# Performance work log

Hardware: AMD Instinct MI355X
Metric: run time of the kernel (lower is better)

## Reference

```python
import jax, jax.numpy as jnp
import numpy as np

H = 1024          # hiddenSize
V = 50257         # outputSize (vocab)
L = 512           # maxLength (encoder length)


def setup_inputs() -> dict:
    key = jax.random.key(0)
    ks = jax.random.split(key, 16)
    s = 0.02
    return {
        "input": jax.random.randint(ks[0], (1,), 0, V),
        "hidden": jax.random.normal(ks[1], (1, 1, H), jnp.float32),
        "encoder_outputs": jax.random.normal(ks[2], (L, H), jnp.float32),
        "emb": jax.random.normal(ks[3], (V, H), jnp.float32) * s,
        "W_attn": jax.random.normal(ks[4], (L, 2 * H), jnp.float32) * s,
        "b_attn": jnp.zeros((L,), jnp.float32),
        "W_comb": jax.random.normal(ks[5], (H, 2 * H), jnp.float32) * s,
        "b_comb": jnp.zeros((H,), jnp.float32),
        "W_ih": jax.random.normal(ks[6], (3 * H, H), jnp.float32) * s,
        "W_hh": jax.random.normal(ks[7], (3 * H, H), jnp.float32) * s,
        "b_ih": jnp.zeros((3 * H,), jnp.float32),
        "b_hh": jnp.zeros((3 * H,), jnp.float32),
        "W_out": jax.random.normal(ks[8], (V, H), jnp.float32) * s,
        "b_out": jnp.zeros((V,), jnp.float32),
    }


def reference(input, hidden, encoder_outputs, emb, W_attn, b_attn,
              W_comb, b_comb, W_ih, W_hh, b_ih, b_hh, W_out, b_out):
    # embedding lookup: [1, H] (dropout p=0 -> identity)
    embedded = emb[input]
    h = hidden[0]                                   # [1, H]
    # attention over encoder positions
    attn_logits = jnp.concatenate([embedded, h], axis=1) @ W_attn.T + b_attn
    attn_weights = jax.nn.softmax(attn_logits, axis=1)      # [1, L]
    attn_applied = attn_weights @ encoder_outputs           # [1, H]
    # combine and relu
    x = jnp.concatenate([embedded, attn_applied], axis=1) @ W_comb.T + b_comb
    x = jax.nn.relu(x)                                      # [1, H]
    # single GRU step (PyTorch gate layout: r, z, n)
    gi = x @ W_ih.T + b_ih                                  # [1, 3H]
    gh = h @ W_hh.T + b_hh                                  # [1, 3H]
    i_r, i_z, i_n = jnp.split(gi, 3, axis=1)
    h_r, h_z, h_n = jnp.split(gh, 3, axis=1)
    r = jax.nn.sigmoid(i_r + h_r)
    z = jax.nn.sigmoid(i_z + h_z)
    n = jnp.tanh(i_n + r * h_n)
    h_new = (1.0 - z) * n + z * h                           # [1, H]
    # output distribution
    output = jax.nn.log_softmax(h_new @ W_out.T + b_out, axis=1)  # [1, V]
    return output, h_new[None], attn_weights
```

## Files before the change

kernel.cpp:

```cpp
#include <hip/hip_runtime.h>
#include <cmath>

#define H 1024
#define V 50257
#define L 512
#define NB5 1571
#define NPART 128

__device__ __forceinline__ float wred_sum(float v) {
#pragma unroll
    for (int o = 32; o > 0; o >>= 1) v += __shfl_xor(v, o, 64);
    return v;
}
__device__ __forceinline__ float dot4(float4 a, float4 b) {
    return a.x * b.x + a.y * b.y + a.z * b.z + a.w * b.w;
}
__device__ __forceinline__ void ms_merge(float& m, float& s, float m2, float s2) {
    float M = fmaxf(m, m2);
    if (M == -INFINITY) { m = M; s = 0.f; return; }
    s = s * expf(m - M) + s2 * expf(m2 - M);
    m = M;
}

__global__ void k_phase1(const int* __restrict__ tok,
                         const float* __restrict__ hid,
                         const float* __restrict__ emb,
                         const float* __restrict__ Wa,
                         const float* __restrict__ ba,
                         const float* __restrict__ enc,
                         const float* __restrict__ Whh,
                         const float* __restrict__ bhh,
                         float* __restrict__ elg,
                         float* __restrict__ pbuf,
                         float* __restrict__ gh) {
    const int t = threadIdx.x, lane = t & 63, wv = t >> 6, b = blockIdx.x;
    const float4* h4 = (const float4*)hid;
    if (b < NPART) {
        const int l = b * 4 + wv;
        const float4* e4 = (const float4*)(emb + (size_t)tok[0] * H);
        const float4* wr = (const float4*)(Wa + (size_t)l * 2048);
        float acc = 0.f;
#pragma unroll
        for (int k = 0; k < 8; ++k) {
            int f = 64 * k + lane;
            float4 s = (f < 256) ? e4[f] : h4[f - 256];
            acc += dot4(wr[f], s);
        }
        acc = wred_sum(acc);
        const float e = expf(acc + ba[l]);
        __shared__ float se[4];
        if (lane == 0) { se[wv] = e; elg[l] = e; }
        __syncthreads();
        float4 a = make_float4(0.f, 0.f, 0.f, 0.f);
#pragma unroll
        for (int r = 0; r < 4; ++r) {
            const float w = se[r];
            const float4 v = ((const float4*)(enc + (size_t)(b * 4 + r) * H))[t];
            a.x += w * v.x; a.y += w * v.y; a.z += w * v.z; a.w += w * v.w;
        }
        ((float4*)pbuf)[b * 256 + t] = a;
    } else {
        const int base = (b - NPART) * 12 + wv * 3;
#pragma unroll
        for (int r = 0; r < 3; ++r) {
            const int j = base + r;
            const float4* wh = (const float4*)(Whh + (size_t)j * H);
            float acc = 0.f;
#pragma unroll
            for (int k = 0; k < 4; ++k) {
                int f = 64 * k + lane;
                acc += dot4(wh[f], h4[f]);
            }
            acc = wred_sum(acc);
            if (lane == 0) gh[j] = acc + bhh[j];
        }
    }
}

__global__ void k_comb(const int* __restrict__ tok,
                       const float* __restrict__ emb,
                       const float* __restrict__ elg,
                       const float* __restrict__ pbuf,
                       const float* __restrict__ Wc,
                       const float* __restrict__ bcb,
                       float* __restrict__ xv,
                       float* __restrict__ wout) {
    const int t = threadIdx.x, lane = t & 63, wv = t >> 6, b = blockIdx.x;
    __shared__ float red[4];
    __shared__ float4 aaL[256];
    const float e0 = elg[t], e1 = elg[t + 256];
    float s = wred_sum(e0 + e1);
    if (lane == 0) red[wv] = s;
    __syncthreads();
    const float invS = 1.f / (red[0] + red[1] + red[2] + red[3]);
    float4 a = make_float4(0.f, 0.f, 0.f, 0.f);
#pragma unroll 8
    for (int i = 0; i < NPART; ++i) {
        const float4 p = ((const float4*)pbuf)[i * 256 + t];
        a.x += p.x; a.y += p.y; a.z += p.z; a.w += p.w;
    }
    a.x *= invS; a.y *= invS; a.z *= invS; a.w *= invS;
    aaL[t] = a;
    __syncthreads();
    if (b == 0) { wout[t] = e0 * invS; wout[t + 256] = e1 * invS; }
    const int j = b * 4 + wv;
    const float4* e4 = (const float4*)(emb + (size_t)tok[0] * H);
    const float4* wr = (const float4*)(Wc + (size_t)j * 2048);
    float acc = 0.f;
#pragma unroll
    for (int k = 0; k < 4; ++k) {
        int f = 64 * k + lane;
        acc += dot4(wr[f], e4[f]);
        acc += dot4(wr[256 + f], aaL[f]);
    }
    acc = wred_sum(acc);
    if (lane == 0) xv[j] = fmaxf(acc + bcb[j], 0.f);
}

__global__ void k_gates_gru(const float* __restrict__ xv,
                            const float* __restrict__ hid,
                            const float* __restrict__ Wih,
                            const float* __restrict__ bih,
                            const float* __restrict__ gh,
                            float* __restrict__ hn_out,
                            float* __restrict__ hn_ws) {
    const int lane = threadIdx.x & 63, wv = threadIdx.x >> 6;
    const int j = blockIdx.x * 4 + wv;
    const float4* x4 = (const float4*)xv;
    float4 xreg[4];
#pragma unroll
    for (int k = 0; k < 4; ++k) xreg[k] = x4[64 * k + lane];
    float g[3];
#pragma unroll
    for (int p = 0; p < 3; ++p) {
        const float4* wr = (const float4*)(Wih + (size_t)(j + p * H) * H);
        float acc = 0.f;
#pragma unroll
        for (int k = 0; k < 4; ++k) acc += dot4(wr[64 * k + lane], xreg[k]);
        g[p] = wred_sum(acc) + bih[j + p * H];
    }
    if (lane == 0) {
        float r = 1.f / (1.f + expf(-(g[0] + gh[j])));
        float z = 1.f / (1.f + expf(-(g[1] + gh[j + H])));
        float n = tanhf(g[2] + r * gh[j + 2 * H]);
        float hv = (1.f - z) * n + z * hid[j];
        hn_out[j] = hv;
        hn_ws[j] = hv;
    }
}

__global__ void k_out_gemv(const float* __restrict__ hn,
                           const float* __restrict__ Wo,
                           const float* __restrict__ bo,
                           float* __restrict__ logits,
                           float* __restrict__ pm,
                           float* __restrict__ ps) {
    const int lane = threadIdx.x & 63, wv = threadIdx.x >> 6;
    const int b = blockIdx.x;
    const float4* h4 = (const float4*)hn;
    float4 hreg[4];
#pragma unroll
    for (int k = 0; k < 4; ++k) hreg[k] = h4[64 * k + lane];
    float lv[8];
    int nvalid = 0;
#pragma unroll
    for (int i = 0; i < 8; ++i) {
        const int v = b * 32 + wv * 8 + i;
        if (v < V) {
            const float4* wr = (const float4*)(Wo + (size_t)v * H);
            float acc = 0.f;
#pragma unroll
            for (int k = 0; k < 4; ++k) acc += dot4(wr[64 * k + lane], hreg[k]);
            acc = wred_sum(acc) + bo[v];
            if (lane == 0) logits[v] = acc;
            lv[nvalid++] = acc;
        }
    }
    float m = -INFINITY, s = 0.f;
    for (int i = 0; i < nvalid; ++i) m = fmaxf(m, lv[i]);
    for (int i = 0; i < nvalid; ++i) s += expf(lv[i] - m);
    __shared__ float smm[4], sms[4];
    if (lane == 0) { smm[wv] = m; sms[wv] = s; }
    __syncthreads();
    if (threadIdx.x == 0) {
        float M = smm[0], S = sms[0];
#pragma unroll
        for (int i = 1; i < 4; ++i) ms_merge(M, S, smm[i], sms[i]);
        pm[b] = M; ps[b] = S;
    }
}

__global__ void k_finalize(float* __restrict__ out,
                           const float* __restrict__ pm,
                           const float* __restrict__ ps) {
    const int t = threadIdx.x, lane = t & 63, wv = t >> 6;
    float m = -INFINITY, s = 0.f;
    for (int i = t; i < NB5; i += 256) ms_merge(m, s, pm[i], ps[i]);
#pragma unroll
    for (int o = 32; o > 0; o >>= 1) {
        float m2 = __shfl_xor(m, o, 64);
        float s2 = __shfl_xor(s, o, 64);
        ms_merge(m, s, m2, s2);
    }
    __shared__ float smm[4], sms[4];
    __shared__ float Cs;
    if (lane == 0) { smm[wv] = m; sms[wv] = s; }
    __syncthreads();
    if (t == 0) {
        float M = smm[0], S = sms[0];
#pragma unroll
        for (int i = 1; i < 4; ++i) ms_merge(M, S, smm[i], sms[i]);
        Cs = M + logf(S);
    }
    __syncthreads();
    const float C = Cs;
    const int v = blockIdx.x * 256 + t;
    if (v < V) out[v] -= C;
}

extern "C" void kernel_launch(void* const* d_in, const int* in_sizes, int n_in,
                              void* d_out, int out_size, void* d_ws, size_t ws_size,
                              hipStream_t stream) {
    const int*   tok = (const int*)d_in[0];
    const float* hid = (const float*)d_in[1];
    const float* enc = (const float*)d_in[2];
    const float* emb = (const float*)d_in[3];
    const float* Wa  = (const float*)d_in[4];
    const float* ba  = (const float*)d_in[5];
    const float* Wc  = (const float*)d_in[6];
    const float* bc  = (const float*)d_in[7];
    const float* Wih = (const float*)d_in[8];
    const float* Whh = (const float*)d_in[9];
    const float* bih = (const float*)d_in[10];
    const float* bhh = (const float*)d_in[11];
    const float* Wo  = (const float*)d_in[12];
    const float* bo  = (const float*)d_in[13];

    float* out = (float*)d_out;
    float* ws  = (float*)d_ws;
    float* elg  = ws;
    float* gh   = ws + 512;
    float* xv   = ws + 3584;
    float* hn   = ws + 4608;
    float* pm   = ws + 5632;
    float* psum = ws + 7203;
    float* pbuf = ws + 8832;

    float* out_logits = out;
    float* out_hnew   = out + V;
    float* out_attnw  = out + V + H;

    k_phase1<<<384, 256, 0, stream>>>(tok, hid, emb, Wa, ba, enc, Whh, bhh,
                                      elg, pbuf, gh);
    k_comb<<<256, 256, 0, stream>>>(tok, emb, elg, pbuf, Wc, bc, xv, out_attnw);
    k_gates_gru<<<256, 256, 0, stream>>>(xv, hid, Wih, bih, gh, out_hnew, hn);
    k_out_gemv<<<NB5, 256, 0, stream>>>(hn, Wo, bo, out_logits, pm, psum);
    k_finalize<<<197, 256, 0, stream>>>(out_logits, pm, psum);
}
```

Before: 64.61 us.

## Split attention reduction into separate kernel, widen W_hh grid, stream W_out nontemporally

```diff
diff --git a/kernel.cpp b/kernel.cpp
--- a/kernel.cpp
+++ b/kernel.cpp
@@ -7,12 +7,14 @@
 #define NB5 1571
 #define NPART 128
 
+typedef float f4 __attribute__((ext_vector_type(4)));
+
 __device__ __forceinline__ float wred_sum(float v) {
 #pragma unroll
     for (int o = 32; o > 0; o >>= 1) v += __shfl_xor(v, o, 64);
     return v;
 }
-__device__ __forceinline__ float dot4(float4 a, float4 b) {
+__device__ __forceinline__ float dot4f(f4 a, f4 b) {
     return a.x * b.x + a.y * b.y + a.z * b.z + a.w * b.w;
 }
 __device__ __forceinline__ void ms_merge(float& m, float& s, float m2, float s2) {
@@ -34,84 +36,85 @@
                          float* __restrict__ pbuf,
                          float* __restrict__ gh) {
     const int t = threadIdx.x, lane = t & 63, wv = t >> 6, b = blockIdx.x;
-    const float4* h4 = (const float4*)hid;
+    const f4* h4 = (const f4*)hid;
     if (b < NPART) {
         const int l = b * 4 + wv;
-        const float4* e4 = (const float4*)(emb + (size_t)tok[0] * H);
-        const float4* wr = (const float4*)(Wa + (size_t)l * 2048);
+        const f4* e4 = (const f4*)(emb + (size_t)tok[0] * H);
+        const f4* wr = (const f4*)(Wa + (size_t)l * 2048);
         float acc = 0.f;
 #pragma unroll
         for (int k = 0; k < 8; ++k) {
             int f = 64 * k + lane;
-            float4 s = (f < 256) ? e4[f] : h4[f - 256];
-            acc += dot4(wr[f], s);
+            f4 s = (f < 256) ? e4[f] : h4[f - 256];
+            acc += dot4f(wr[f], s);
         }
         acc = wred_sum(acc);
+        __shared__ float se[4];
         const float e = expf(acc + ba[l]);
-        __shared__ float se[4];
         if (lane == 0) { se[wv] = e; elg[l] = e; }
         __syncthreads();
-        float4 a = make_float4(0.f, 0.f, 0.f, 0.f);
-#pragma unroll
-        for (int r = 0; r < 4; ++r) {
-            const float w = se[r];
-            const float4 v = ((const float4*)(enc + (size_t)(b * 4 + r) * H))[t];
-            a.x += w * v.x; a.y += w * v.y; a.z += w * v.z; a.w += w * v.w;
-        }
-        ((float4*)pbuf)[b * 256 + t] = a;
+        f4 a = {0.f, 0.f, 0.f, 0.f};
+#pragma unroll
+        for (int r = 0; r < 4; ++r)
+            a += se[r] * ((const f4*)(enc + (size_t)(b * 4 + r) * H))[t];
+        ((f4*)pbuf)[b * 256 + t] = a;
     } else {
-        const int base = (b - NPART) * 12 + wv * 3;
-#pragma unroll
-        for (int r = 0; r < 3; ++r) {
-            const int j = base + r;
-            const float4* wh = (const float4*)(Whh + (size_t)j * H);
-            float acc = 0.f;
-#pragma unroll
-            for (int k = 0; k < 4; ++k) {
-                int f = 64 * k + lane;
-                acc += dot4(wh[f], h4[f]);
-            }
-            acc = wred_sum(acc);
-            if (lane == 0) gh[j] = acc + bhh[j];
-        }
-    }
+        const int j = (b - NPART) * 4 + wv;
+        const f4* wh = (const f4*)(Whh + (size_t)j * H);
+        float acc = 0.f;
+#pragma unroll
+        for (int k = 0; k < 4; ++k) {
+            int f = 64 * k + lane;
+            acc += dot4f(wh[f], h4[f]);
+        }
+        acc = wred_sum(acc);
+        if (lane == 0) gh[j] = acc + bhh[j];
+    }
+}
+
+__global__ void k_reduce(const float* __restrict__ elg,
+                         const float* __restrict__ pbuf,
+                         float* __restrict__ aa,
+                         float* __restrict__ wout) {
+    const int t = threadIdx.x, b = blockIdx.x;
+    const int g = t >> 6, c = t & 63;
+    __shared__ float red[4];
+    const float e0 = elg[t], e1 = elg[t + 256];
+    float s = wred_sum(e0 + e1);
+    if (c == 0) red[g] = s;
+    __syncthreads();
+    const float invS = 1.f / (red[0] + red[1] + red[2] + red[3]);
+    const int col = b * 64 + c;
+    f4 a = {0.f, 0.f, 0.f, 0.f};
+#pragma unroll 8
+    for (int i = g; i < NPART; i += 4) a += ((const f4*)pbuf)[i * 256 + col];
+    __shared__ f4 racc[4][64];
+    racc[g][c] = a;
+    __syncthreads();
+    if (g == 0) {
+        f4 tot = (racc[0][c] + racc[1][c] + racc[2][c] + racc[3][c]) * invS;
+        ((f4*)aa)[col] = tot;
+    }
+    if (b == 0) { wout[t] = e0 * invS; wout[t + 256] = e1 * invS; }
 }
 
 __global__ void k_comb(const int* __restrict__ tok,
                        const float* __restrict__ emb,
-                       const float* __restrict__ elg,
-                       const float* __restrict__ pbuf,
+                       const float* __restrict__ aa,
                        const float* __restrict__ Wc,
                        const float* __restrict__ bcb,
-                       float* __restrict__ xv,
-                       float* __restrict__ wout) {
-    const int t = threadIdx.x, lane = t & 63, wv = t >> 6, b = blockIdx.x;
-    __shared__ float red[4];
-    __shared__ float4 aaL[256];
-    const float e0 = elg[t], e1 = elg[t + 256];
-    float s = wred_sum(e0 + e1);
-    if (lane == 0) red[wv] = s;
-    __syncthreads();
-    const float invS = 1.f / (red[0] + red[1] + red[2] + red[3]);
-    float4 a = make_float4(0.f, 0.f, 0.f, 0.f);
-#pragma unroll 8
-    for (int i = 0; i < NPART; ++i) {
-        const float4 p = ((const float4*)pbuf)[i * 256 + t];
-        a.x += p.x; a.y += p.y; a.z += p.z; a.w += p.w;
-    }
-    a.x *= invS; a.y *= invS; a.z *= invS; a.w *= invS;
-    aaL[t] = a;
-    __syncthreads();
-    if (b == 0) { wout[t] = e0 * invS; wout[t + 256] = e1 * invS; }
-    const int j = b * 4 + wv;
-    const float4* e4 = (const float4*)(emb + (size_t)tok[0] * H);
-    const float4* wr = (const float4*)(Wc + (size_t)j * 2048);
+                       float* __restrict__ xv) {
+    const int lane = threadIdx.x & 63, wv = threadIdx.x >> 6;
+    const int j = blockIdx.x * 4 + wv;
+    const f4* e4 = (const f4*)(emb + (size_t)tok[0] * H);
+    const f4* a4 = (const f4*)aa;
+    const f4* wr = (const f4*)(Wc + (size_t)j * 2048);
     float acc = 0.f;
 #pragma unroll
     for (int k = 0; k < 4; ++k) {
         int f = 64 * k + lane;
-        acc += dot4(wr[f], e4[f]);
-        acc += dot4(wr[256 + f], aaL[f]);
+        acc += dot4f(wr[f], e4[f]);
+        acc += dot4f(wr[256 + f], a4[f]);
     }
     acc = wred_sum(acc);
     if (lane == 0) xv[j] = fmaxf(acc + bcb[j], 0.f);
@@ -126,17 +129,17 @@
                             float* __restrict__ hn_ws) {
     const int lane = threadIdx.x & 63, wv = threadIdx.x >> 6;
     const int j = blockIdx.x * 4 + wv;
-    const float4* x4 = (const float4*)xv;
-    float4 xreg[4];
+    const f4* x4 = (const f4*)xv;
+    f4 xreg[4];
 #pragma unroll
     for (int k = 0; k < 4; ++k) xreg[k] = x4[64 * k + lane];
     float g[3];
 #pragma unroll
     for (int p = 0; p < 3; ++p) {
-        const float4* wr = (const float4*)(Wih + (size_t)(j + p * H) * H);
+        const f4* wr = (const f4*)(Wih + (size_t)(j + p * H) * H);
         float acc = 0.f;
 #pragma unroll
-        for (int k = 0; k < 4; ++k) acc += dot4(wr[64 * k + lane], xreg[k]);
+        for (int k = 0; k < 4; ++k) acc += dot4f(wr[64 * k + lane], xreg[k]);
         g[p] = wred_sum(acc) + bih[j + p * H];
     }
     if (lane == 0) {
@@ -157,28 +160,47 @@
                            float* __restrict__ ps) {
     const int lane = threadIdx.x & 63, wv = threadIdx.x >> 6;
     const int b = blockIdx.x;
-    const float4* h4 = (const float4*)hn;
-    float4 hreg[4];
+    const int rbase = b * 32 + wv * 8;
+    const f4* h4 = (const f4*)hn;
+    f4 hreg[4];
 #pragma unroll
     for (int k = 0; k < 4; ++k) hreg[k] = h4[64 * k + lane];
-    float lv[8];
-    int nvalid = 0;
-#pragma unroll
-    for (int i = 0; i < 8; ++i) {
-        const int v = b * 32 + wv * 8 + i;
-        if (v < V) {
-            const float4* wr = (const float4*)(Wo + (size_t)v * H);
+    float m = -INFINITY, s = 0.f;
+    if (b != NB5 - 1) {
+        float lv[8];
+#pragma unroll
+        for (int i = 0; i < 8; ++i) {
+            const f4* wr = (const f4*)(Wo + (size_t)(rbase + i) * H);
             float acc = 0.f;
 #pragma unroll
-            for (int k = 0; k < 4; ++k) acc += dot4(wr[64 * k + lane], hreg[k]);
-            acc = wred_sum(acc) + bo[v];
-            if (lane == 0) logits[v] = acc;
-            lv[nvalid++] = acc;
-        }
-    }
-    float m = -INFINITY, s = 0.f;
-    for (int i = 0; i < nvalid; ++i) m = fmaxf(m, lv[i]);
-    for (int i = 0; i < nvalid; ++i) s += expf(lv[i] - m);
+            for (int k = 0; k < 4; ++k)
+                acc += dot4f(__builtin_nontemporal_load(wr + 64 * k + lane), hreg[k]);
+            acc = wred_sum(acc) + bo[rbase + i];
+            if (lane == 0) logits[rbase + i] = acc;
+            lv[i] = acc;
+        }
+#pragma unroll
+        for (int i = 0; i < 8; ++i) m = fmaxf(m, lv[i]);
+#pragma unroll
+        for (int i = 0; i < 8; ++i) s += expf(lv[i] - m);
+    } else {
+#pragma unroll
+        for (int i = 0; i < 8; ++i) {
+            const int v = rbase + i;
+            if (v < V) {
+                const f4* wr = (const f4*)(Wo + (size_t)v * H);
+                float acc = 0.f;
+#pragma unroll
+                for (int k = 0; k < 4; ++k)
+                    acc += dot4f(__builtin_nontemporal_load(wr + 64 * k + lane), hreg[k]);
+                acc = wred_sum(acc) + bo[v];
+                if (lane == 0) logits[v] = acc;
+                float M = fmaxf(m, acc);
+                s = s * expf(m - M) + expf(acc - M);
+                m = M;
+            }
+        }
+    }
     __shared__ float smm[4], sms[4];
     if (lane == 0) { smm[wv] = m; sms[wv] = s; }
     __syncthreads();
@@ -240,19 +262,21 @@
     float* ws  = (float*)d_ws;
     float* elg  = ws;
     float* gh   = ws + 512;
-    float* xv   = ws + 3584;
-    float* hn   = ws + 4608;
-    float* pm   = ws + 5632;
-    float* psum = ws + 7203;
-    float* pbuf = ws + 8832;
+    float* aa   = ws + 3584;
+    float* xv   = ws + 4608;
+    float* hn   = ws + 5632;
+    float* pm   = ws + 6656;
+    float* psum = ws + 8256;
+    float* pbuf = ws + 9856;
 
     float* out_logits = out;
     float* out_hnew   = out + V;
     float* out_attnw  = out + V + H;
 
-    k_phase1<<<384, 256, 0, stream>>>(tok, hid, emb, Wa, ba, enc, Whh, bhh,
-                                      elg, pbuf, gh);
-    k_comb<<<256, 256, 0, stream>>>(tok, emb, elg, pbuf, Wc, bc, xv, out_attnw);
+    k_phase1<<<NPART + 768, 256, 0, stream>>>(tok, hid, emb, Wa, ba, enc, Whh, bhh,
+                                              elg, pbuf, gh);
+    k_reduce<<<4, 256, 0, stream>>>(elg, pbuf, aa, out_attnw);
+    k_comb<<<256, 256, 0, stream>>>(tok, emb, aa, Wc, bc, xv);
     k_gates_gru<<<256, 256, 0, stream>>>(xv, hid, Wih, bih, gh, out_hnew, hn);
     k_out_gemv<<<NB5, 256, 0, stream>>>(hn, Wo, bo, out_logits, pm, psum);
     k_finalize<<<197, 256, 0, stream>>>(out_logits, pm, psum);
```

Result: faster. 61.27 us (-5.2%).
